# Kernel tuning notes

Measured on AMD Instinct MI355X. Metric: run time of the kernel, lower is better.

## Reference

```python
import jax, jax.numpy as jnp
import numpy as np
import math

HIDDEN = 2048
HEADS = 16
GROUPS = 4
HEAD_DIM = HIDDEN // HEADS  # 128
KV_DIM = GROUPS * HEAD_DIM  # 512
B, S = 2, 2048


def setup_inputs() -> dict:
    key = jax.random.key(0)
    ks = jax.random.split(key, 10)
    scale = 0.02
    return {
        "X": jax.random.normal(ks[0], (B, S, HIDDEN), dtype=jnp.float32),
        "attention_mask": jnp.ones((B, S), dtype=jnp.int32),
        "Wq": jax.random.normal(ks[1], (HIDDEN, HIDDEN), dtype=jnp.float32) * scale,
        "bq": jnp.zeros((HIDDEN,), dtype=jnp.float32),
        "Wk": jax.random.normal(ks[2], (HIDDEN, KV_DIM), dtype=jnp.float32) * scale,
        "bk": jnp.zeros((KV_DIM,), dtype=jnp.float32),
        "Wv": jax.random.normal(ks[3], (HIDDEN, KV_DIM), dtype=jnp.float32) * scale,
        "bv": jnp.zeros((KV_DIM,), dtype=jnp.float32),
        "Wo": jax.random.normal(ks[4], (HIDDEN, HIDDEN), dtype=jnp.float32) * scale,
        "bo": jnp.zeros((HIDDEN,), dtype=jnp.float32),
    }


def reference(X, attention_mask, Wq, bq, Wk, bk, Wv, bv, Wo, bo):
    b, s, _ = X.shape
    num_per_group = HEADS // GROUPS
    # projections
    Q = (X @ Wq + bq).reshape(b, s, HEADS, HEAD_DIM).transpose(0, 2, 1, 3)   # [b,H,s,d]
    K = (X @ Wk + bk).reshape(b, s, GROUPS, HEAD_DIM).transpose(0, 2, 1, 3)  # [b,G,s,d]
    V = (X @ Wv + bv).reshape(b, s, GROUPS, HEAD_DIM).transpose(0, 2, 1, 3)
    # torch .repeat(1, num_per_group, 1, 1) tiles group axis: [g0..gG-1, g0..gG-1, ...]
    K = jnp.tile(K, (1, num_per_group, 1, 1))  # [b,H,s,d]
    V = jnp.tile(V, (1, num_per_group, 1, 1))
    scores = jnp.einsum("bhqd,bhkd->bhqk", Q, K) / math.sqrt(HEAD_DIM)
    mask = attention_mask[:, None, None, :] == 0  # [b,1,1,s]
    scores = jnp.where(mask, jnp.float32(-jnp.inf), scores)
    attn = jax.nn.softmax(scores, axis=-1)
    out = jnp.einsum("bhqk,bhkd->bhqd", attn, V)  # [b,H,s,d]
    out = out.transpose(0, 2, 1, 3).reshape(b, s, HIDDEN)
    return out @ Wo + bo
```

## Files before the change

kernel.cpp:

```cpp
#include <hip/hip_runtime.h>
#include <hip/hip_bf16.h>


typedef __attribute__((ext_vector_type(8))) short short8;
typedef __attribute__((ext_vector_type(4))) short short4v;
typedef __attribute__((ext_vector_type(4))) float float4v;

#define C1F 0.12751743f
#define B0F -16.0f

#if defined(__has_builtin) && __has_builtin(__builtin_amdgcn_exp2f)
#define EXP2(x) __builtin_amdgcn_exp2f(x)
#else
#define EXP2(x) exp2f(x)
#endif

__device__ __forceinline__ short f2bf(float x) {
    __hip_bfloat16 h = __float2bfloat16(x);
    short s; __builtin_memcpy(&s, &h, sizeof(s)); return s;
}

__device__ __forceinline__ void gl16(const short* g, short* l) {
    __builtin_amdgcn_global_load_lds(
        (const __attribute__((address_space(1))) void*)g,
        (__attribute__((address_space(3))) void*)l, 16, 0, 0);
}

__global__ __launch_bounds__(256) void cvt_bf16_kernel(const float* __restrict__ in,
                                                       short* __restrict__ out, int n) {
    int i = (blockIdx.x * 256 + threadIdx.x) * 4;
    if (i >= n) return;
    float4 v = *(const float4*)(in + i);
    short4v o;
    o[0] = f2bf(v.x); o[1] = f2bf(v.y); o[2] = f2bf(v.z); o[3] = f2bf(v.w);
    *(short4v*)(out + i) = o;
}

__global__ __launch_bounds__(256) void transpose_cvt_kernel(const float* __restrict__ W,
                                                            short* __restrict__ Wt,
                                                            int K, int N) {
    __shared__ float tile[32][33];
    int n0 = blockIdx.x * 32, k0 = blockIdx.y * 32;
    int tx = threadIdx.x & 31, ty = threadIdx.x >> 5;
#pragma unroll
    for (int i = 0; i < 4; ++i) {
        int kk = ty + i * 8;
        tile[kk][tx] = W[(size_t)(k0 + kk) * N + n0 + tx];
    }
    __syncthreads();
#pragma unroll
    for (int i = 0; i < 4; ++i) {
        int nn = ty + i * 8;
        Wt[(size_t)(n0 + nn) * K + k0 + tx] = f2bf(tile[tx][nn]);
    }
}

__global__ __launch_bounds__(256) void gemm_dma_kernel(
    const short* __restrict__ A, const short* __restrict__ Bt,
    const float* __restrict__ b0, const float* __restrict__ b1, const float* __restrict__ b2,
    short* __restrict__ O0, short* __restrict__ O1, short* __restrict__ O2,
    float* __restrict__ Of, int K, int mode) {
    __shared__ short As[128 * 32];
    __shared__ short Bs[128 * 32];
    const int t = threadIdx.x, lane = t & 63, w = t >> 6;
    const int l15 = lane & 15, quad = lane >> 4;
    const int wm = (w & 1) * 64, wn = (w >> 1) * 64;
    const int m0 = blockIdx.y * 128, n0 = blockIdx.x * 128;
    const int r4 = lane >> 2, c8 = (lane & 3) * 8;
    const short* ga = A + (size_t)(m0 + w * 16 + r4) * K + c8;
    const short* gb = Bt + (size_t)(n0 + w * 16 + r4) * K + c8;
    short* lA = As + (w * 16) * 32;
    short* lB = Bs + (w * 16) * 32;

    float4v acc[4][4] = {};

    for (int k0 = 0; k0 < K; k0 += 32) {
        gl16(ga + k0, lA);
        gl16(ga + (size_t)64 * K + k0, lA + 64 * 32);
        gl16(gb + k0, lB);
        gl16(gb + (size_t)64 * K + k0, lB + 64 * 32);
        __syncthreads();
        short8 af[4], bfr[4];
#pragma unroll
        for (int i = 0; i < 4; ++i)
            af[i] = *(const short8*)(As + (wm + i * 16 + l15) * 32 + quad * 8);
#pragma unroll
        for (int j = 0; j < 4; ++j)
            bfr[j] = *(const short8*)(Bs + (wn + j * 16 + l15) * 32 + quad * 8);
#pragma unroll
        for (int i = 0; i < 4; ++i)
#pragma unroll
            for (int j = 0; j < 4; ++j)
                acc[i][j] = __builtin_amdgcn_mfma_f32_16x16x32_bf16(af[i], bfr[j], acc[i][j], 0, 0, 0);
        __syncthreads();
    }

#pragma unroll
    for (int i = 0; i < 4; ++i) {
#pragma unroll
        for (int j = 0; j < 4; ++j) {
            const int col = n0 + wn + j * 16 + l15;
            const int row0 = m0 + wm + i * 16 + quad * 4;
            if (mode == 1) {
                const float bc = b0[col];
#pragma unroll
                for (int r = 0; r < 4; ++r)
                    Of[(size_t)(row0 + r) * 2048 + col] = acc[i][j][r] + bc;
            } else if (col < 2048) {
                const float bc = b0[col];
#pragma unroll
                for (int r = 0; r < 4; ++r)
                    O0[(size_t)(row0 + r) * 2048 + col] = f2bf(acc[i][j][r] + bc);
            } else if (col < 2560) {
                const int c = col - 2048;
                const float bc = b1[c];
#pragma unroll
                for (int r = 0; r < 4; ++r)
                    O1[(size_t)(row0 + r) * 512 + c] = f2bf(acc[i][j][r] + bc);
            } else {
                const int c = col - 2560;
                const float bc = b2[c];
#pragma unroll
                for (int r = 0; r < 4; ++r)
                    O2[(size_t)c * 4096 + row0 + r] = f2bf(acc[i][j][r] + bc);
            }
        }
    }
}

__global__ __launch_bounds__(512, 2) void flash_kernel(
    const short* __restrict__ Qb, const short* __restrict__ Kb,
    const short* __restrict__ Vt, const int* __restrict__ mask,
    short* __restrict__ Ab) {
    __shared__ short Ks[64 * 136];
    __shared__ short Vs[128 * 72];
    __shared__ short Ps[8 * 32 * 72];
    __shared__ float mb[64];

    const int t = threadIdx.x;
    const int lane = t & 63, w = t >> 6;
    const int l15 = lane & 15, quad = lane >> 4;
    const int qt = blockIdx.x, g = blockIdx.y, b = blockIdx.z;
    const int h = g + 4 * (w & 3);
    const int q0 = qt * 64 + (w >> 2) * 32;

    short8 qf[2][4];
#pragma unroll
    for (int mi = 0; mi < 2; ++mi)
#pragma unroll
        for (int ks = 0; ks < 4; ++ks)
            qf[mi][ks] = *(const short8*)(Qb + (size_t)(b * 2048 + q0 + mi * 16 + l15) * 2048
                                          + h * 128 + ks * 32 + quad * 8);

    float4v o[2][8] = {};
    float rsum[2][4] = {};
    short* PsW = Ps + w * (32 * 72);

    const int kR = t >> 4, kC = (t & 15) * 8;
    const int vR = t >> 3, vC = (t & 7) * 8;
    const short* kg = Kb + (size_t)(b * 2048 + kR) * 512 + g * 128 + kC;
    const short* vg = Vt + (size_t)(g * 128 + vR) * 4096 + (size_t)b * 2048 + vC;

    for (int kt = 0; kt < 32; ++kt) {
        const int kb = kt * 64;
        short8 k0v = *(const short8*)(kg + (size_t)kb * 512);
        short8 k1v = *(const short8*)(kg + (size_t)(kb + 32) * 512);
        short8 v0v = *(const short8*)(vg + kb);
        short8 v1v = *(const short8*)(vg + (size_t)64 * 4096 + kb);
        float mv = 0.f;
        if (t < 64) mv = mask[b * 2048 + kb + t] ? B0F : -1e30f;
        __syncthreads();
        *(short8*)(Ks + kR * 136 + kC) = k0v;
        *(short8*)(Ks + (kR + 32) * 136 + kC) = k1v;
        *(short8*)(Vs + vR * 72 + vC) = v0v;
        *(short8*)(Vs + (vR + 64) * 72 + vC) = v1v;
        if (t < 64) mb[t] = mv;
        __syncthreads();

        float4v s[2][4] = {};
#pragma unroll
        for (int ks = 0; ks < 4; ++ks)
#pragma unroll
            for (int j = 0; j < 4; ++j) {
                short8 bk = *(const short8*)(Ks + (j * 16 + l15) * 136 + ks * 32 + quad * 8);
                s[0][j] = __builtin_amdgcn_mfma_f32_16x16x32_bf16(qf[0][ks], bk, s[0][j], 0, 0, 0);
                s[1][j] = __builtin_amdgcn_mfma_f32_16x16x32_bf16(qf[1][ks], bk, s[1][j], 0, 0, 0);
            }
#pragma unroll
        for (int mi = 0; mi < 2; ++mi)
#pragma unroll
            for (int j = 0; j < 4; ++j) {
                const float mbias = mb[j * 16 + l15];
#pragma unroll
                for (int r = 0; r < 4; ++r) {
                    float p = EXP2(fmaf(s[mi][j][r], C1F, mbias));
                    rsum[mi][r] += p;
                    PsW[(mi * 16 + quad * 4 + r) * 72 + j * 16 + l15] = f2bf(p);
                }
            }
#pragma unroll
        for (int ks2 = 0; ks2 < 2; ++ks2) {
            short8 pa0 = *(const short8*)(PsW + l15 * 72 + ks2 * 32 + quad * 8);
            short8 pa1 = *(const short8*)(PsW + (16 + l15) * 72 + ks2 * 32 + quad * 8);
#pragma unroll
            for (int jj = 0; jj < 8; ++jj) {
                short8 bv = *(const short8*)(Vs + (jj * 16 + l15) * 72 + ks2 * 32 + quad * 8);
                o[0][jj] = __builtin_amdgcn_mfma_f32_16x16x32_bf16(pa0, bv, o[0][jj], 0, 0, 0);
                o[1][jj] = __builtin_amdgcn_mfma_f32_16x16x32_bf16(pa1, bv, o[1][jj], 0, 0, 0);
            }
        }
    }

    float rinv[2][4];
#pragma unroll
    for (int mi = 0; mi < 2; ++mi)
#pragma unroll
        for (int r = 0; r < 4; ++r) {
            float v = rsum[mi][r];
            v += __shfl_xor(v, 1, 64); v += __shfl_xor(v, 2, 64);
            v += __shfl_xor(v, 4, 64); v += __shfl_xor(v, 8, 64);
            rinv[mi][r] = (v > 0.f) ? 1.f / v : 0.f;
        }
    const size_t ob = (size_t)(b * 2048 + q0) * 2048 + h * 128;
#pragma unroll
    for (int mi = 0; mi < 2; ++mi)
#pragma unroll
        for (int jj = 0; jj < 8; ++jj)
#pragma unroll
            for (int r = 0; r < 4; ++r)
                Ab[ob + (size_t)(mi * 16 + quad * 4 + r) * 2048 + jj * 16 + l15] =
                    f2bf(o[mi][jj][r] * rinv[mi][r]);
}

extern "C" void kernel_launch(void* const* d_in, const int* in_sizes, int n_in,
                              void* d_out, int out_size, void* d_ws, size_t ws_size,
                              hipStream_t stream) {
    (void)in_sizes; (void)n_in; (void)out_size; (void)ws_size;
    const float* X  = (const float*)d_in[0];
    const int* mask = (const int*)d_in[1];
    const float* Wq = (const float*)d_in[2];
    const float* bq = (const float*)d_in[3];
    const float* Wk = (const float*)d_in[4];
    const float* bk = (const float*)d_in[5];
    const float* Wv = (const float*)d_in[6];
    const float* bv = (const float*)d_in[7];
    const float* Wo = (const float*)d_in[8];
    const float* bo = (const float*)d_in[9];
    float* out = (float*)d_out;

    char* ws = (char*)d_ws;
    short* Xb     = (short*)(ws + 0);
    short* WqkvT  = (short*)(ws + 16777216);
    short* Wot    = (short*)(ws + 29360128);
    short* Qb     = (short*)(ws + 37748736);
    short* Kb     = (short*)(ws + 54525952);
    short* Vt     = (short*)(ws + 58720256);
    short* Ab     = Xb;

    const int M = 4096, HID = 2048, KV = 512;

    cvt_bf16_kernel<<<8192, 256, 0, stream>>>(X, Xb, M * HID);
    transpose_cvt_kernel<<<dim3(64, 64), 256, 0, stream>>>(Wq, WqkvT, HID, HID);
    transpose_cvt_kernel<<<dim3(16, 64), 256, 0, stream>>>(Wk, WqkvT + (size_t)2048 * 2048, HID, KV);
    transpose_cvt_kernel<<<dim3(16, 64), 256, 0, stream>>>(Wv, WqkvT + (size_t)2560 * 2048, HID, KV);
    transpose_cvt_kernel<<<dim3(64, 64), 256, 0, stream>>>(Wo, Wot, HID, HID);

    gemm_dma_kernel<<<dim3(24, 32), 256, 0, stream>>>(
        Xb, WqkvT, bq, bk, bv, Qb, Kb, Vt, nullptr, HID, 0);

    flash_kernel<<<dim3(32, 4, 2), 512, 0, stream>>>(Qb, Kb, Vt, mask, Ab);

    gemm_dma_kernel<<<dim3(16, 32), 256, 0, stream>>>(
        Ab, Wot, bo, nullptr, nullptr, nullptr, nullptr, nullptr, out, HID, 1);
}
```

Before: 346.0 us.

## Shrink flash blocks to 4 waves over 32 queries and pad P tile stride

The flash attention kernel now runs 256-thread blocks covering 32 query rows for the four heads of a KV group, doubling the grid to 512 blocks. Each thread loads four K and four V vectors per tile instead of two. The P staging buffer stride is padded from 72 to 76 to reduce LDS bank conflicts, with reads split into two 4-wide loads. K fragments are also batched into registers before the MFMAs. Smaller blocks improve occupancy and load balance, but each K/V tile is now loaded by twice as many blocks, doubling global K/V traffic, and the split reads add LDS instructions.

```diff
diff --git a/kernel.cpp b/kernel.cpp
--- a/kernel.cpp
+++ b/kernel.cpp
@@ -128,21 +128,23 @@
     }
 }
 
-__global__ __launch_bounds__(512, 2) void flash_kernel(
+#define PSTR 76
+
+__global__ __launch_bounds__(256, 2) void flash_kernel(
     const short* __restrict__ Qb, const short* __restrict__ Kb,
     const short* __restrict__ Vt, const int* __restrict__ mask,
     short* __restrict__ Ab) {
     __shared__ short Ks[64 * 136];
     __shared__ short Vs[128 * 72];
-    __shared__ short Ps[8 * 32 * 72];
+    __shared__ short Ps[4 * 32 * PSTR];
     __shared__ float mb[64];
 
     const int t = threadIdx.x;
     const int lane = t & 63, w = t >> 6;
     const int l15 = lane & 15, quad = lane >> 4;
     const int qt = blockIdx.x, g = blockIdx.y, b = blockIdx.z;
-    const int h = g + 4 * (w & 3);
-    const int q0 = qt * 64 + (w >> 2) * 32;
+    const int h = g + 4 * w;
+    const int q0 = qt * 32;
 
     short8 qf[2][4];
 #pragma unroll
@@ -154,7 +156,7 @@
 
     float4v o[2][8] = {};
     float rsum[2][4] = {};
-    short* PsW = Ps + w * (32 * 72);
+    short* PsW = Ps + w * (32 * PSTR);
 
     const int kR = t >> 4, kC = (t & 15) * 8;
     const int vR = t >> 3, vC = (t & 7) * 8;
@@ -163,29 +165,41 @@
 
     for (int kt = 0; kt < 32; ++kt) {
         const int kb = kt * 64;
-        short8 k0v = *(const short8*)(kg + (size_t)kb * 512);
-        short8 k1v = *(const short8*)(kg + (size_t)(kb + 32) * 512);
-        short8 v0v = *(const short8*)(vg + kb);
-        short8 v1v = *(const short8*)(vg + (size_t)64 * 4096 + kb);
+        short8 kv0 = *(const short8*)(kg + (size_t)(kb +  0) * 512);
+        short8 kv1 = *(const short8*)(kg + (size_t)(kb + 16) * 512);
+        short8 kv2 = *(const short8*)(kg + (size_t)(kb + 32) * 512);
+        short8 kv3 = *(const short8*)(kg + (size_t)(kb + 48) * 512);
+        short8 vv0 = *(const short8*)(vg + (size_t)  0 * 4096 + kb);
+        short8 vv1 = *(const short8*)(vg + (size_t) 32 * 4096 + kb);
+        short8 vv2 = *(const short8*)(vg + (size_t) 64 * 4096 + kb);
+        short8 vv3 = *(const short8*)(vg + (size_t) 96 * 4096 + kb);
         float mv = 0.f;
         if (t < 64) mv = mask[b * 2048 + kb + t] ? B0F : -1e30f;
         __syncthreads();
-        *(short8*)(Ks + kR * 136 + kC) = k0v;
-        *(short8*)(Ks + (kR + 32) * 136 + kC) = k1v;
-        *(short8*)(Vs + vR * 72 + vC) = v0v;
-        *(short8*)(Vs + (vR + 64) * 72 + vC) = v1v;
+        *(short8*)(Ks + (kR +  0) * 136 + kC) = kv0;
+        *(short8*)(Ks + (kR + 16) * 136 + kC) = kv1;
+        *(short8*)(Ks + (kR + 32) * 136 + kC) = kv2;
+        *(short8*)(Ks + (kR + 48) * 136 + kC) = kv3;
+        *(short8*)(Vs + (vR +  0) * 72 + vC) = vv0;
+        *(short8*)(Vs + (vR + 32) * 72 + vC) = vv1;
+        *(short8*)(Vs + (vR + 64) * 72 + vC) = vv2;
+        *(short8*)(Vs + (vR + 96) * 72 + vC) = vv3;
         if (t < 64) mb[t] = mv;
         __syncthreads();
 
         float4v s[2][4] = {};
 #pragma unroll
-        for (int ks = 0; ks < 4; ++ks)
+        for (int ks = 0; ks < 4; ++ks) {
+            short8 bk[4];
+#pragma unroll
+            for (int j = 0; j < 4; ++j)
+                bk[j] = *(const short8*)(Ks + (j * 16 + l15) * 136 + ks * 32 + quad * 8);
 #pragma unroll
             for (int j = 0; j < 4; ++j) {
-                short8 bk = *(const short8*)(Ks + (j * 16 + l15) * 136 + ks * 32 + quad * 8);
-                s[0][j] = __builtin_amdgcn_mfma_f32_16x16x32_bf16(qf[0][ks], bk, s[0][j], 0, 0, 0);
-                s[1][j] = __builtin_amdgcn_mfma_f32_16x16x32_bf16(qf[1][ks], bk, s[1][j], 0, 0, 0);
-            }
+                s[0][j] = __builtin_amdgcn_mfma_f32_16x16x32_bf16(qf[0][ks], bk[j], s[0][j], 0, 0, 0);
+                s[1][j] = __builtin_amdgcn_mfma_f32_16x16x32_bf16(qf[1][ks], bk[j], s[1][j], 0, 0, 0);
+            }
+        }
 #pragma unroll
         for (int mi = 0; mi < 2; ++mi)
 #pragma unroll
@@ -195,18 +209,25 @@
                 for (int r = 0; r < 4; ++r) {
                     float p = EXP2(fmaf(s[mi][j][r], C1F, mbias));
                     rsum[mi][r] += p;
-                    PsW[(mi * 16 + quad * 4 + r) * 72 + j * 16 + l15] = f2bf(p);
+                    PsW[(mi * 16 + quad * 4 + r) * PSTR + j * 16 + l15] = f2bf(p);
                 }
             }
 #pragma unroll
         for (int ks2 = 0; ks2 < 2; ++ks2) {
-            short8 pa0 = *(const short8*)(PsW + l15 * 72 + ks2 * 32 + quad * 8);
-            short8 pa1 = *(const short8*)(PsW + (16 + l15) * 72 + ks2 * 32 + quad * 8);
+            short8 pa[2];
+#pragma unroll
+            for (int mi = 0; mi < 2; ++mi) {
+                const short* pp = PsW + (mi * 16 + l15) * PSTR + ks2 * 32 + quad * 8;
+                short4v lo = *(const short4v*)(pp);
+                short4v hi = *(const short4v*)(pp + 4);
+                pa[mi][0] = lo[0]; pa[mi][1] = lo[1]; pa[mi][2] = lo[2]; pa[mi][3] = lo[3];
+                pa[mi][4] = hi[0]; pa[mi][5] = hi[1]; pa[mi][6] = hi[2]; pa[mi][7] = hi[3];
+            }
 #pragma unroll
             for (int jj = 0; jj < 8; ++jj) {
                 short8 bv = *(const short8*)(Vs + (jj * 16 + l15) * 72 + ks2 * 32 + quad * 8);
-                o[0][jj] = __builtin_amdgcn_mfma_f32_16x16x32_bf16(pa0, bv, o[0][jj], 0, 0, 0);
-                o[1][jj] = __builtin_amdgcn_mfma_f32_16x16x32_bf16(pa1, bv, o[1][jj], 0, 0, 0);
+                o[0][jj] = __builtin_amdgcn_mfma_f32_16x16x32_bf16(pa[0], bv, o[0][jj], 0, 0, 0);
+                o[1][jj] = __builtin_amdgcn_mfma_f32_16x16x32_bf16(pa[1], bv, o[1][jj], 0, 0, 0);
             }
         }
     }
@@ -268,7 +289,7 @@
     gemm_dma_kernel<<<dim3(24, 32), 256, 0, stream>>>(
         Xb, WqkvT, bq, bk, bv, Qb, Kb, Vt, nullptr, HID, 0);
 
-    flash_kernel<<<dim3(32, 4, 2), 512, 0, stream>>>(Qb, Kb, Vt, mask, Ab);
+    flash_kernel<<<dim3(64, 4, 2), 256, 0, stream>>>(Qb, Kb, Vt, mask, Ab);
 
     gemm_dma_kernel<<<dim3(16, 32), 256, 0, stream>>>(
         Ab, Wot, bo, nullptr, nullptr, nullptr, nullptr, nullptr, out, HID, 1);
```

New measurement: 346.6 us. About the same (+0.2%).
